# Kernel optimization log

Measured on AMD Instinct MI355X. Metric: run time of the kernel, lower is better.

The kernel has to match this reference:

```python
import jax, jax.numpy as jnp
import numpy as np

EPS = 1e-5


def setup_inputs() -> dict:
    key = jax.random.key(0)
    ks = jax.random.split(key, 6)
    B, H, W, C = 4, 64, 64, 64
    x_in = jax.random.normal(ks[0], (B, H, W, C), dtype=jnp.float32)
    scale = 1.0 / np.sqrt(C)
    w1 = jax.random.normal(ks[1], (C, C), dtype=jnp.float32) * scale
    w2 = jax.random.normal(ks[2], (C, C), dtype=jnp.float32) * scale
    w3 = jax.random.normal(ks[3], (C, C), dtype=jnp.float32) * scale
    w4 = jax.random.normal(ks[4], (C, C), dtype=jnp.float32) * scale
    zeros = jnp.zeros((C,), dtype=jnp.float32)
    return {
        "x_in": x_in,
        "w1": w1, "w2": w2, "w3": w3, "w4": w4,
        "b1": zeros, "b2": zeros, "b3": zeros, "b4": zeros,
        "gamma": jnp.ones((C,), dtype=jnp.float32),
        "beta": zeros,
    }


def reference(x_in, w1, w2, w3, w4, b1, b2, b3, b4, gamma, beta):
    B, H, W, C = x_in.shape
    # BatchNorm over batch + spatial dims, per channel (training-mode batch stats)
    mean = jnp.mean(x_in, axis=(0, 1, 2))            # [C]
    var = jnp.var(x_in, axis=(0, 1, 2))              # [C]
    x = (x_in - mean) * jax.lax.rsqrt(var + EPS) * gamma + beta
    # QKV projections
    q = jnp.einsum('bhwc,cC->bhwC', x, w1) + b1
    k = jnp.einsum('bhwc,cC->bhwC', x, w2) + b2
    v = jnp.einsum('bhwc,cC->bhwC', x, w3) + b3
    # Full spatial attention: [B, H, W, H, W]
    sdpa = jnp.einsum('bhwc,bHWc->bhwHW', q, k) / jnp.sqrt(jnp.float32(C))
    sdpa = jax.nn.softmax(sdpa.reshape(B, H, W, H * W), axis=-1)
    sdpa = sdpa.reshape(B, H, W, H, W)
    x = jnp.einsum('bhwHW,bHWc->bhwc', sdpa, v)
    # Output projection + residual
    x = jnp.einsum('bhwc,cC->bhwC', x, w4) + b4
    return x + x_in
```

## Files before the change

kernel.cpp:

```cpp
#include <hip/hip_runtime.h>

typedef _Float16 f16;
typedef _Float16 half8 __attribute__((ext_vector_type(8)));
typedef float f32x4 __attribute__((ext_vector_type(4)));

#define LDW 72

__global__ __launch_bounds__(256) void k_bnstats(const float* __restrict__ x, float* __restrict__ sums){
    __shared__ float red[512];
    int t = threadIdx.x;
    int c = t & 63, rg = t >> 6;
    int rb = blockIdx.x * 64;
    float s = 0.f, s2 = 0.f;
    for(int r = rg; r < 64; r += 4){
        float v = x[(rb + r) * 64 + c];
        s += v; s2 += v * v;
    }
    red[t] = s; red[256 + t] = s2;
    __syncthreads();
    if(t < 64){
        float a = red[t] + red[t + 64] + red[t + 128] + red[t + 192];
        float b = red[256 + t] + red[256 + t + 64] + red[256 + t + 128] + red[256 + t + 192];
        atomicAdd(&sums[c], a);
        atomicAdd(&sums[64 + c], b);
    }
}

__global__ __launch_bounds__(256) void k_qkv(
    const float* __restrict__ x,
    const float* __restrict__ w1, const float* __restrict__ w2, const float* __restrict__ w3,
    const float* __restrict__ b1, const float* __restrict__ b2, const float* __restrict__ b3,
    const float* __restrict__ gamma, const float* __restrict__ beta,
    const float* __restrict__ sums,
    f16* __restrict__ Q, f16* __restrict__ Kx, f16* __restrict__ Vt){
    __shared__ f16 wT[3 * 64 * LDW];
    __shared__ float sc[64], sh[64], bb[3][64];
    int t = threadIdx.x;
    for(int i = t; i < 3 * 4096; i += 256){
        int j = i >> 12, e = i & 4095, k = e >> 6, n = e & 63;
        const float* wp = (j == 0) ? w1 : ((j == 1) ? w2 : w3);
        wT[j * 64 * LDW + n * LDW + k] = (f16)wp[e];
    }
    if(t < 64){
        float mean = sums[t] * (1.f / 16384.f);
        float var  = sums[64 + t] * (1.f / 16384.f) - mean * mean;
        float s = gamma[t] * rsqrtf(var + 1e-5f);
        sc[t] = s;
        sh[t] = beta[t] - mean * s;
        bb[0][t] = b1[t]; bb[1][t] = b2[t]; bb[2][t] = b3[t];
    }
    __syncthreads();
    int w = t >> 6, lane = t & 63, quad = lane >> 4, l15 = lane & 15;
    int rowb = blockIdx.x * 64 + w * 16;
    int arow = rowb + l15;
    half8 a[2];
    #pragma unroll
    for(int kc = 0; kc < 2; kc++){
        f32x4 x0 = *(const f32x4*)&x[arow * 64 + kc * 32 + quad * 8];
        f32x4 x1 = *(const f32x4*)&x[arow * 64 + kc * 32 + quad * 8 + 4];
        half8 h;
        #pragma unroll
        for(int j = 0; j < 8; j++){
            int c = kc * 32 + quad * 8 + j;
            float xv = (j < 4) ? x0[j & 3] : x1[j & 3];
            h[j] = (f16)(xv * sc[c] + sh[c]);
        }
        a[kc] = h;
    }
    const f32x4 vzero = {0.f, 0.f, 0.f, 0.f};
    f32x4 acc[3][4];
    #pragma unroll
    for(int m = 0; m < 3; m++){
        #pragma unroll
        for(int nt = 0; nt < 4; nt++){
            acc[m][nt] = vzero;
            #pragma unroll
            for(int kc = 0; kc < 2; kc++){
                half8 bfr = *(half8*)&wT[m * 64 * LDW + (nt * 16 + l15) * LDW + kc * 32 + quad * 8];
                acc[m][nt] = __builtin_amdgcn_mfma_f32_16x16x32_f16(a[kc], bfr, acc[m][nt], 0, 0, 0);
            }
        }
    }
    const float qs = 0.18033688011112043f;
    #pragma unroll
    for(int nt = 0; nt < 4; nt++){
        #pragma unroll
        for(int r = 0; r < 4; r++){
            int row = rowb + quad * 4 + r;
            int col = nt * 16 + l15;
            Q[row * 64 + col]  = (f16)((acc[0][nt][r] + bb[0][col]) * qs);
            Kx[row * 64 + col] = (f16)(acc[1][nt][r] + bb[1][col]);
            Vt[((row >> 12) * 64 + col) * 4096 + (row & 4095)] = (f16)(acc[2][nt][r] + bb[2][col]);
        }
    }
}

__global__ __launch_bounds__(256, 2) void k_attn(
    const f16* __restrict__ Q, const f16* __restrict__ Kx, const f16* __restrict__ Vt,
    f16* __restrict__ Oph, float* __restrict__ lw){
    __shared__ f16 Ks[64 * LDW];
    __shared__ f16 Vs[64 * LDW];
    __shared__ f16 Pw[4][16 * LDW];
    int t = threadIdx.x;
    int kq = blockIdx.x & 7, qg = blockIdx.x >> 3;
    int b = qg >> 4;
    int w = t >> 6, lane = t & 63, quad = lane >> 4, l15 = lane & 15;
    int qrow0 = qg * 256 + w * 64;

    half8 aq[4][2];
    #pragma unroll
    for(int rg = 0; rg < 4; rg++)
        #pragma unroll
        for(int kc = 0; kc < 2; kc++)
            aq[rg][kc] = *(const half8*)&Q[(qrow0 + rg * 16 + l15) * 64 + kc * 32 + quad * 8];

    const f16* gsrc[4];
    f16* ldst[4];
    int gstep[4];
    #pragma unroll
    for(int i = 0; i < 4; i++){
        int idx = t + i * 256;
        int rr = (idx >> 3) & 63;
        int c8 = idx & 7;
        int kt0 = kq * 8;
        if(idx < 512){
            ldst[i] = &Ks[rr * LDW + c8 * 8];
            gsrc[i] = &Kx[(b * 4096 + kt0 * 64 + rr) * 64 + c8 * 8];
            gstep[i] = 64 * 64;
        } else {
            ldst[i] = &Vs[rr * LDW + c8 * 8];
            gsrc[i] = &Vt[(b * 64 + rr) * 4096 + kt0 * 64 + c8 * 8];
            gstep[i] = 64;
        }
    }
    half8 pre[4];
    #pragma unroll
    for(int i = 0; i < 4; i++){ pre[i] = *(const half8*)gsrc[i]; gsrc[i] += gstep[i]; }

    const f32x4 vzero = {0.f, 0.f, 0.f, 0.f};
    f32x4 o[4][4];
    float lp[4][4];
    #pragma unroll
    for(int rg = 0; rg < 4; rg++)
        #pragma unroll
        for(int nt = 0; nt < 4; nt++){ o[rg][nt] = vzero; lp[rg][nt] = 0.f; }

    for(int j = 0; j < 8; j++){
        __syncthreads();
        #pragma unroll
        for(int i = 0; i < 4; i++) *(half8*)ldst[i] = pre[i];
        __syncthreads();
        if(j < 7){
            #pragma unroll
            for(int i = 0; i < 4; i++){ pre[i] = *(const half8*)gsrc[i]; gsrc[i] += gstep[i]; }
        }
        half8 kf[4][2], vf[4][2];
        #pragma unroll
        for(int nt = 0; nt < 4; nt++)
            #pragma unroll
            for(int kc = 0; kc < 2; kc++){
                kf[nt][kc] = *(half8*)&Ks[(nt * 16 + l15) * LDW + kc * 32 + quad * 8];
                vf[nt][kc] = *(half8*)&Vs[(nt * 16 + l15) * LDW + kc * 32 + quad * 8];
            }
        #pragma unroll
        for(int rg = 0; rg < 4; rg++){
            f32x4 s[4];
            #pragma unroll
            for(int nt = 0; nt < 4; nt++){
                s[nt] = vzero;
                #pragma unroll
                for(int kc = 0; kc < 2; kc++)
                    s[nt] = __builtin_amdgcn_mfma_f32_16x16x32_f16(aq[rg][kc], kf[nt][kc], s[nt], 0, 0, 0);
            }
            #pragma unroll
            for(int nt = 0; nt < 4; nt++){
                #pragma unroll
                for(int r = 0; r < 4; r++){
                    float p = __builtin_amdgcn_exp2f(fminf(s[nt][r], 15.f));
                    lp[rg][r] += p;
                    Pw[w][(quad * 4 + r) * LDW + nt * 16 + l15] = (f16)p;
                }
            }
            #pragma unroll
            for(int kc = 0; kc < 2; kc++){
                half8 pf = *(half8*)&Pw[w][l15 * LDW + kc * 32 + quad * 8];
                #pragma unroll
                for(int nt = 0; nt < 4; nt++)
                    o[rg][nt] = __builtin_amdgcn_mfma_f32_16x16x32_f16(pf, vf[nt][kc], o[rg][nt], 0, 0, 0);
            }
        }
    }
    #pragma unroll
    for(int rg = 0; rg < 4; rg++){
        #pragma unroll
        for(int r = 0; r < 4; r++){
            float v = lp[rg][r];
            v += __shfl_xor(v, 1); v += __shfl_xor(v, 2);
            v += __shfl_xor(v, 4); v += __shfl_xor(v, 8);
            int row = qrow0 + rg * 16 + quad * 4 + r;
            if(l15 == 0) lw[kq * 16384 + row] = v;
            float inv = __builtin_amdgcn_rcpf(v);
            #pragma unroll
            for(int nt = 0; nt < 4; nt++)
                Oph[kq * 1048576 + row * 64 + nt * 16 + l15] = (f16)(o[rg][nt][r] * inv);
        }
    }
}

__global__ __launch_bounds__(256) void k_merge(
    const f16* __restrict__ Oph, const float* __restrict__ lw,
    const float* __restrict__ w4, const float* __restrict__ b4,
    const float* __restrict__ x, float* __restrict__ out){
    __shared__ f16 Om[64 * LDW];
    __shared__ f16 wT[64 * LDW];
    __shared__ float b4f[64];
    int t = threadIdx.x;
    int rb = blockIdx.x * 64;
    for(int i = t; i < 4096; i += 256){
        int k = i >> 6, n = i & 63;
        wT[n * LDW + k] = (f16)w4[i];
    }
    if(t < 64) b4f[t] = b4[t];
    for(int i = t; i < 512; i += 256){
        int row = i >> 3, c8 = i & 7;
        int gr = rb + row;
        float num[8] = {0.f,0.f,0.f,0.f,0.f,0.f,0.f,0.f};
        float den = 0.f;
        #pragma unroll
        for(int s = 0; s < 8; s++){
            float li = lw[s * 16384 + gr];
            half8 ov = *(const half8*)&Oph[s * 1048576 + gr * 64 + c8 * 8];
            #pragma unroll
            for(int j = 0; j < 8; j++) num[j] += li * (float)ov[j];
            den += li;
        }
        float invd = 1.f / den;
        #pragma unroll
        for(int j = 0; j < 8; j++) Om[row * LDW + c8 * 8 + j] = (f16)(num[j] * invd);
    }
    __syncthreads();
    int w = t >> 6, lane = t & 63, quad = lane >> 4, l15 = lane & 15;
    half8 a[2];
    #pragma unroll
    for(int kc = 0; kc < 2; kc++)
        a[kc] = *(half8*)&Om[(w * 16 + l15) * LDW + kc * 32 + quad * 8];
    #pragma unroll
    for(int nt = 0; nt < 4; nt++){
        f32x4 y = {0.f, 0.f, 0.f, 0.f};
        #pragma unroll
        for(int kc = 0; kc < 2; kc++){
            half8 bfr = *(half8*)&wT[(nt * 16 + l15) * LDW + kc * 32 + quad * 8];
            y = __builtin_amdgcn_mfma_f32_16x16x32_f16(a[kc], bfr, y, 0, 0, 0);
        }
        #pragma unroll
        for(int r = 0; r < 4; r++){
            int row = rb + w * 16 + quad * 4 + r;
            int col = nt * 16 + l15;
            out[row * 64 + col] = y[r] + b4f[col] + x[row * 64 + col];
        }
    }
}

extern "C" void kernel_launch(void* const* d_in, const int* in_sizes, int n_in,
                              void* d_out, int out_size, void* d_ws, size_t ws_size,
                              hipStream_t stream){
    (void)in_sizes; (void)n_in; (void)out_size; (void)ws_size;
    const float* x  = (const float*)d_in[0];
    const float* w1 = (const float*)d_in[1];
    const float* w2 = (const float*)d_in[2];
    const float* w3 = (const float*)d_in[3];
    const float* w4 = (const float*)d_in[4];
    const float* b1 = (const float*)d_in[5];
    const float* b2 = (const float*)d_in[6];
    const float* b3 = (const float*)d_in[7];
    const float* b4 = (const float*)d_in[8];
    const float* gm = (const float*)d_in[9];
    const float* bt = (const float*)d_in[10];
    char* ws = (char*)d_ws;
    f16* Q   = (f16*)(ws);
    f16* Kx  = (f16*)(ws + (size_t)(2u << 20));
    f16* Vt  = (f16*)(ws + (size_t)(4u << 20));
    float* sums = (float*)(ws + (size_t)(6u << 20));
    f16* Oph = (f16*)(ws + (size_t)(6u << 20) + 1024);
    float* lwp = (float*)(ws + (size_t)(22u << 20) + 1024);

    hipMemsetAsync(sums, 0, 512, stream);
    hipLaunchKernelGGL(k_bnstats, dim3(256), dim3(256), 0, stream, x, sums);
    hipLaunchKernelGGL(k_qkv,     dim3(256), dim3(256), 0, stream, x, w1, w2, w3, b1, b2, b3, gm, bt, sums, Q, Kx, Vt);
    hipLaunchKernelGGL(k_attn,    dim3(512), dim3(256), 0, stream, Q, Kx, Vt, Oph, lwp);
    hipLaunchKernelGGL(k_merge,   dim3(256), dim3(256), 0, stream, Oph, lwp, w4, b4, x, (float*)d_out);
}
```

Before: 140.5 us.

## Use 32x32x16 MFMA with register-resident P and double-buffered K/V

```diff
diff --git a/kernel.cpp b/kernel.cpp
--- a/kernel.cpp
+++ b/kernel.cpp
@@ -1,8 +1,11 @@
 #include <hip/hip_runtime.h>
 
 typedef _Float16 f16;
+typedef _Float16 half2 __attribute__((ext_vector_type(2)));
 typedef _Float16 half8 __attribute__((ext_vector_type(8)));
 typedef float f32x4 __attribute__((ext_vector_type(4)));
+typedef float f32x16 __attribute__((ext_vector_type(16)));
+typedef unsigned u32x4 __attribute__((ext_vector_type(4)));
 
 #define LDW 72
 
@@ -98,37 +101,33 @@
 __global__ __launch_bounds__(256, 2) void k_attn(
     const f16* __restrict__ Q, const f16* __restrict__ Kx, const f16* __restrict__ Vt,
     f16* __restrict__ Oph, float* __restrict__ lw){
-    __shared__ f16 Ks[64 * LDW];
-    __shared__ f16 Vs[64 * LDW];
-    __shared__ f16 Pw[4][16 * LDW];
+    __shared__ f16 KV[2][2 * 64 * LDW];
+    __shared__ float lred[4][64];
     int t = threadIdx.x;
     int kq = blockIdx.x & 7, qg = blockIdx.x >> 3;
     int b = qg >> 4;
-    int w = t >> 6, lane = t & 63, quad = lane >> 4, l15 = lane & 15;
+    int w = t >> 6, lane = t & 63, l31 = lane & 31, hi = lane >> 5;
     int qrow0 = qg * 256 + w * 64;
 
-    half8 aq[4][2];
-    #pragma unroll
-    for(int rg = 0; rg < 4; rg++)
-        #pragma unroll
-        for(int kc = 0; kc < 2; kc++)
-            aq[rg][kc] = *(const half8*)&Q[(qrow0 + rg * 16 + l15) * 64 + kc * 32 + quad * 8];
+    half8 aq[2][4];
+    #pragma unroll
+    for(int qt = 0; qt < 2; qt++)
+        #pragma unroll
+        for(int dc = 0; dc < 4; dc++)
+            aq[qt][dc] = *(const half8*)&Q[(qrow0 + qt * 32 + l31) * 64 + dc * 16 + hi * 8];
 
     const f16* gsrc[4];
-    f16* ldst[4];
-    int gstep[4];
+    int loff[4], gstep[4];
     #pragma unroll
     for(int i = 0; i < 4; i++){
         int idx = t + i * 256;
-        int rr = (idx >> 3) & 63;
-        int c8 = idx & 7;
-        int kt0 = kq * 8;
+        int rr = (idx >> 3) & 63, c8 = idx & 7, kt0 = kq * 8;
         if(idx < 512){
-            ldst[i] = &Ks[rr * LDW + c8 * 8];
+            loff[i] = rr * LDW + c8 * 8;
             gsrc[i] = &Kx[(b * 4096 + kt0 * 64 + rr) * 64 + c8 * 8];
             gstep[i] = 64 * 64;
         } else {
-            ldst[i] = &Vs[rr * LDW + c8 * 8];
+            loff[i] = 64 * LDW + rr * LDW + c8 * 8;
             gsrc[i] = &Vt[(b * 64 + rr) * 4096 + kt0 * 64 + c8 * 8];
             gstep[i] = 64;
         }
@@ -136,75 +135,102 @@
     half8 pre[4];
     #pragma unroll
     for(int i = 0; i < 4; i++){ pre[i] = *(const half8*)gsrc[i]; gsrc[i] += gstep[i]; }
-
-    const f32x4 vzero = {0.f, 0.f, 0.f, 0.f};
-    f32x4 o[4][4];
-    float lp[4][4];
-    #pragma unroll
-    for(int rg = 0; rg < 4; rg++)
-        #pragma unroll
-        for(int nt = 0; nt < 4; nt++){ o[rg][nt] = vzero; lp[rg][nt] = 0.f; }
-
+    #pragma unroll
+    for(int i = 0; i < 4; i++) *(half8*)&KV[0][loff[i]] = pre[i];
+
+    f32x16 o[2][2];
+    #pragma unroll
+    for(int qt = 0; qt < 2; qt++)
+        #pragma unroll
+        for(int dt = 0; dt < 2; dt++)
+            #pragma unroll
+            for(int r = 0; r < 16; r++) o[qt][dt][r] = 0.f;
+    float lp[2] = {0.f, 0.f};
+
+    __syncthreads();
+    int cur = 0;
     for(int j = 0; j < 8; j++){
-        __syncthreads();
-        #pragma unroll
-        for(int i = 0; i < 4; i++) *(half8*)ldst[i] = pre[i];
-        __syncthreads();
         if(j < 7){
             #pragma unroll
             for(int i = 0; i < 4; i++){ pre[i] = *(const half8*)gsrc[i]; gsrc[i] += gstep[i]; }
         }
-        half8 kf[4][2], vf[4][2];
-        #pragma unroll
-        for(int nt = 0; nt < 4; nt++)
-            #pragma unroll
-            for(int kc = 0; kc < 2; kc++){
-                kf[nt][kc] = *(half8*)&Ks[(nt * 16 + l15) * LDW + kc * 32 + quad * 8];
-                vf[nt][kc] = *(half8*)&Vs[(nt * 16 + l15) * LDW + kc * 32 + quad * 8];
-            }
-        #pragma unroll
-        for(int rg = 0; rg < 4; rg++){
-            f32x4 s[4];
-            #pragma unroll
-            for(int nt = 0; nt < 4; nt++){
-                s[nt] = vzero;
-                #pragma unroll
-                for(int kc = 0; kc < 2; kc++)
-                    s[nt] = __builtin_amdgcn_mfma_f32_16x16x32_f16(aq[rg][kc], kf[nt][kc], s[nt], 0, 0, 0);
-            }
-            #pragma unroll
-            for(int nt = 0; nt < 4; nt++){
-                #pragma unroll
-                for(int r = 0; r < 4; r++){
-                    float p = __builtin_amdgcn_exp2f(fminf(s[nt][r], 15.f));
-                    lp[rg][r] += p;
-                    Pw[w][(quad * 4 + r) * LDW + nt * 16 + l15] = (f16)p;
+        const f16* Kb = &KV[cur][0];
+        const f16* Vb = &KV[cur][64 * LDW];
+        #pragma unroll
+        for(int kt = 0; kt < 2; kt++){
+            half8 ak[4];
+            #pragma unroll
+            for(int dc = 0; dc < 4; dc++)
+                ak[dc] = *(const half8*)&Kb[(kt * 32 + l31) * LDW + dc * 16 + hi * 8];
+            half8 vb[2][2];
+            #pragma unroll
+            for(int kc = 0; kc < 2; kc++)
+                #pragma unroll
+                for(int dt = 0; dt < 2; dt++)
+                    vb[kc][dt] = *(const half8*)&Vb[(dt * 32 + l31) * LDW + kt * 32 + kc * 16 + hi * 8];
+            #pragma unroll
+            for(int qt = 0; qt < 2; qt++){
+                f32x16 s;
+                #pragma unroll
+                for(int r = 0; r < 16; r++) s[r] = 0.f;
+                #pragma unroll
+                for(int dc = 0; dc < 4; dc++)
+                    s = __builtin_amdgcn_mfma_f32_32x32x16_f16(ak[dc], aq[qt][dc], s, 0, 0, 0);
+                float pf[16], ls = 0.f;
+                #pragma unroll
+                for(int r = 0; r < 16; r++){
+                    float p = __builtin_amdgcn_exp2f(fminf(s[r], 15.f));
+                    pf[r] = p; ls += p;
+                }
+                lp[qt] += ls;
+                unsigned wv[4][2];
+                #pragma unroll
+                for(int g = 0; g < 4; g++){
+                    wv[g][0] = __builtin_bit_cast(unsigned, __builtin_amdgcn_cvt_pkrtz(pf[4*g+0], pf[4*g+1]));
+                    wv[g][1] = __builtin_bit_cast(unsigned, __builtin_amdgcn_cvt_pkrtz(pf[4*g+2], pf[4*g+3]));
+                }
+                #pragma unroll
+                for(int kc = 0; kc < 2; kc++){
+                    unsigned x0 = wv[2*kc][0], y0 = wv[2*kc+1][0];
+                    unsigned x1 = wv[2*kc][1], y1 = wv[2*kc+1][1];
+                    asm("v_permlane32_swap_b32 %0, %1" : "+v"(x0), "+v"(y0));
+                    asm("v_permlane32_swap_b32 %0, %1" : "+v"(x1), "+v"(y1));
+                    u32x4 pw = {x0, x1, y0, y1};
+                    half8 pa = __builtin_bit_cast(half8, pw);
+                    #pragma unroll
+                    for(int dt = 0; dt < 2; dt++)
+                        o[qt][dt] = __builtin_amdgcn_mfma_f32_32x32x16_f16(pa, vb[kc][dt], o[qt][dt], 0, 0, 0);
                 }
             }
-            #pragma unroll
-            for(int kc = 0; kc < 2; kc++){
-                half8 pf = *(half8*)&Pw[w][l15 * LDW + kc * 32 + quad * 8];
-                #pragma unroll
-                for(int nt = 0; nt < 4; nt++)
-                    o[rg][nt] = __builtin_amdgcn_mfma_f32_16x16x32_f16(pf, vf[nt][kc], o[rg][nt], 0, 0, 0);
-            }
-        }
-    }
-    #pragma unroll
-    for(int rg = 0; rg < 4; rg++){
-        #pragma unroll
-        for(int r = 0; r < 4; r++){
-            float v = lp[rg][r];
-            v += __shfl_xor(v, 1); v += __shfl_xor(v, 2);
-            v += __shfl_xor(v, 4); v += __shfl_xor(v, 8);
-            int row = qrow0 + rg * 16 + quad * 4 + r;
-            if(l15 == 0) lw[kq * 16384 + row] = v;
-            float inv = __builtin_amdgcn_rcpf(v);
-            #pragma unroll
-            for(int nt = 0; nt < 4; nt++)
-                Oph[kq * 1048576 + row * 64 + nt * 16 + l15] = (f16)(o[rg][nt][r] * inv);
-        }
-    }
+        }
+        if(j < 7){
+            f16* wb = &KV[cur ^ 1][0];
+            #pragma unroll
+            for(int i = 0; i < 4; i++) *(half8*)(wb + loff[i]) = pre[i];
+        }
+        cur ^= 1;
+        __syncthreads();
+    }
+    #pragma unroll
+    for(int qt = 0; qt < 2; qt++){
+        float v = lp[qt] + __shfl_xor(lp[qt], 32);
+        if(hi == 0){
+            int row = qrow0 + qt * 32 + l31;
+            lw[kq * 16384 + row] = v;
+            lred[w][qt * 32 + l31] = __builtin_amdgcn_rcpf(v);
+        }
+    }
+    #pragma unroll
+    for(int qt = 0; qt < 2; qt++)
+        #pragma unroll
+        for(int r = 0; r < 16; r++){
+            int qrl = qt * 32 + (r & 3) + 8 * (r >> 2) + 4 * hi;
+            float inv = lred[w][qrl];
+            int row = qrow0 + qrl;
+            #pragma unroll
+            for(int dt = 0; dt < 2; dt++)
+                Oph[kq * 1048576 + row * 64 + dt * 32 + l31] = (f16)(o[qt][dt][r] * inv);
+        }
 }
 
 __global__ __launch_bounds__(256) void k_merge(
```

After: 136.3 us. -3.0%, faster.
